# Kernel tuning notes

Hardware: AMD Instinct MI355X
Metric: run time of the kernel (lower is better)

Reference implementation:

```python
import jax, jax.numpy as jnp
import numpy as np

CCA_W, INTRA_W, AUX_W, OS_W, RFS_W = 0.1, 0.05, 1.0, 1.0, 1.0


def cox_loss(risk, events, times):
    # Efron-tied Cox partial likelihood, vectorized over tie groups.
    order = jnp.argsort(-times)  # descending time
    r = risk[order]
    e = events[order]
    t = times[order]
    B = r.shape[0]
    max_r = jnp.max(r)
    exp_r = jnp.exp(r - max_r)
    cum = jnp.cumsum(exp_r)  # risk-set sums (descending time => cumsum)
    # contiguous tie groups (times sorted, ties adjacent)
    new_grp = jnp.concatenate([jnp.zeros(1, jnp.int32), (t[1:] != t[:-1]).astype(jnp.int32)])
    gid = jnp.cumsum(new_grp)
    rss = jax.ops.segment_max(cum, gid, num_segments=B)[gid]          # cum_exp_risk at last idx of group
    tes = jax.ops.segment_sum(exp_r * e, gid, num_segments=B)[gid]     # tied exp-risk sum
    d = jax.ops.segment_sum(e, gid, num_segments=B)[gid]               # tie count (events)
    # rank l of each event within its tie group (0..d-1)
    c = jnp.cumsum(e)
    start = jax.ops.segment_min(jnp.arange(B), gid, num_segments=B)[gid]
    before = c[start] - e[start]
    l = c - 1.0 - before
    d_safe = jnp.where(d > 0, d, 1.0)
    denom = rss - (l / d_safe) * tes
    contrib = e * (r - jnp.log(denom + 1e-12) - max_r)
    n_events = jnp.sum(e)
    return -jnp.sum(contrib) / (n_events + 1e-12)


def distance_correlation_loss(za, zb):
    def dist(x):
        xx = jnp.sum(x * x, axis=1, keepdims=True)
        d2 = xx + xx.T - 2.0 * (x @ x.T)
        return jnp.sqrt(jnp.maximum(d2, 1e-8))
    def dc(D):
        return D - D.mean(axis=1, keepdims=True) - D.mean(axis=0, keepdims=True) + D.mean()
    A = dc(dist(za))
    Bm = dc(dist(zb))
    dcov = jnp.mean(A * Bm)
    va = jnp.mean(A * A)
    vb = jnp.mean(Bm * Bm)
    return 1.0 - dcov / jnp.sqrt(jnp.maximum(va * vb, 1e-8))


def setup_inputs() -> dict:
    key = jax.random.key(0)
    ks = jax.random.split(key, 10)
    B, D = 8192, 256
    return {
        'risk_os': jax.random.normal(ks[0], (B,), jnp.float32),
        'risk_rfs': jax.random.normal(ks[1], (B,), jnp.float32),
        'z_ct': jax.random.normal(ks[2], (B, D), jnp.float32),
        'z_wsi': jax.random.normal(ks[3], (B, D), jnp.float32),
        'intra_wsi': jax.random.uniform(ks[4], (), jnp.float32),
        'intra_ct': jax.random.uniform(ks[5], (), jnp.float32),
        'evt_os': jax.random.randint(ks[6], (B,), 0, 2, jnp.int32),
        'tm_os': jax.random.randint(ks[7], (B,), 0, 1000, jnp.int32),
        'evt_rfs': jax.random.randint(ks[8], (B,), 0, 2, jnp.int32),
        'tm_rfs': jax.random.randint(ks[9], (B,), 0, 1000, jnp.int32),
    }


def reference(risk_os, risk_rfs, z_ct, z_wsi, intra_wsi, intra_ct,
              evt_os, tm_os, evt_rfs, tm_rfs):
    l_os = cox_loss(risk_os, evt_os.astype(jnp.float32), tm_os.astype(jnp.float32))
    l_rfs = cox_loss(risk_rfs, evt_rfs.astype(jnp.float32), tm_rfs.astype(jnp.float32))
    l_cca = distance_correlation_loss(z_ct, z_wsi)
    l_intra = intra_wsi + intra_ct
    total = OS_W * l_os + RFS_W * l_rfs + AUX_W * (CCA_W * l_cca + INTRA_W * l_intra)
    return total
```

## Files before the change

kernel.cpp:

```cpp
#include <hip/hip_runtime.h>
#include <hip/hip_bf16.h>
#include <math.h>

typedef __attribute__((ext_vector_type(4))) float f32x4;
typedef __attribute__((ext_vector_type(4))) int int4v;

#define NBINS 1000

__device__ __forceinline__ void gl16(const void* g, void* l) {
  __builtin_amdgcn_global_load_lds(
      (const __attribute__((address_space(1))) unsigned int*)g,
      (__attribute__((address_space(3))) unsigned int*)l, 16, 0, 0);
}

__device__ __forceinline__ float fp8mag(unsigned b) {
  const int e = (b >> 3) & 15;
  const int m = b & 7;
  return e ? ldexpf((float)(8 + m), e - 10) : ldexpf((float)m, -9);
}

__global__ __launch_bounds__(256)
void prep_kernel(const float* __restrict__ za, const float* __restrict__ zb,
                 float* __restrict__ na, float* __restrict__ nb,
                 unsigned char* __restrict__ zpa, unsigned char* __restrict__ zpb,
                 int B, int D)
{
  const int row = blockIdx.x * 4 + (threadIdx.x >> 6);
  const int lane = threadIdx.x & 63;
  const float* src; float* dst; unsigned char* bd; int r;
  if (row < B) { src = za; dst = na; bd = zpa; r = row; }
  else         { src = zb; dst = nb; bd = zpb; r = row - B; }
  const int rr = r & 127;
  const int sw = (rr >> 1) & 3;
  const size_t tbase = (size_t)(r >> 7) * 128 * D;
  float s = 0.f;
  for (int c = lane * 4; c < D; c += 256) {
    const f32x4 v = *(const f32x4*)&src[(size_t)r * D + c];
    unsigned u = (unsigned)__builtin_amdgcn_cvt_pk_fp8_f32(v[0], v[1], 0, false);
    u = (unsigned)__builtin_amdgcn_cvt_pk_fp8_f32(v[2], v[3], (int)u, true);
    const int sc = c >> 6;
    const int half = (c >> 5) & 1;
    const int kg = (c >> 3) & 3;
    const int rem = c & 7;
    const int slot = kg ^ sw;
    *(unsigned*)&bd[tbase + sc * 8192 + rr * 64 + slot * 16 + half * 8 + rem] = u;
    const float x0 = fp8mag(u & 255), x1 = fp8mag((u >> 8) & 255);
    const float x2 = fp8mag((u >> 16) & 255), x3 = fp8mag(u >> 24);
    s += x0 * x0 + x1 * x1 + x2 * x2 + x3 * x3;
  }
#pragma unroll
  for (int off = 32; off; off >>= 1) s += __shfl_xor(s, off);
  if (lane == 0) dst[r] = s;
}

__global__ __launch_bounds__(512, 2)
void dcor_kernel(const unsigned char* __restrict__ zpa,
                 const unsigned char* __restrict__ zpb,
                 const float* __restrict__ na, const float* __restrict__ nb,
                 float* __restrict__ Ra, float* __restrict__ Rb,
                 double* __restrict__ scalPart,
                 const float* __restrict__ r0, const int* __restrict__ e0, const int* __restrict__ t0,
                 const float* __restrict__ r1, const int* __restrict__ e1, const int* __restrict__ t1,
                 float* __restrict__ coxo,
                 int nt, int B, int D)
{
  __shared__ __align__(16) union SU {
    unsigned char jbuf[2][16384];
    struct { float sS[NBINS], sT[NBINS], sDc[NBINS], sc0[NBINS], sc1[NBINS], red[16], red3[48]; } c;
  } u;

  const int tid = threadIdx.x;
  const int bid = blockIdx.x;

  if (bid < 2) {
    const float* risk = bid ? r1 : r0;
    const int* evt = bid ? e1 : e0;
    const int* tm  = bid ? t1 : t0;
    const int NT = 512;

    float m = -3.0e38f;
    for (int i = tid; i < B; i += NT) m = fmaxf(m, risk[i]);
#pragma unroll
    for (int off = 32; off; off >>= 1) m = fmaxf(m, __shfl_xor(m, off));
    if ((tid & 63) == 0) u.c.red[tid >> 6] = m;
    __syncthreads();
    if (tid == 0) {
      float mm = u.c.red[0];
      for (int wv = 1; wv < 8; ++wv) mm = fmaxf(mm, u.c.red[wv]);
      u.c.red[0] = mm;
    }
    __syncthreads();
    const float maxr = u.c.red[0];

    for (int i = tid; i < NBINS; i += NT) { u.c.sS[i] = 0.f; u.c.sT[i] = 0.f; u.c.sDc[i] = 0.f; }
    __syncthreads();

    float sr = 0.f, nev = 0.f;
    for (int i = tid; i < B; i += NT) {
      const float r = risk[i];
      int t = tm[i];
      t = t < 0 ? 0 : (t >= NBINS ? NBINS - 1 : t);
      const float ex = expf(r - maxr);
      atomicAdd(&u.c.sS[t], ex);
      if (evt[i]) {
        atomicAdd(&u.c.sT[t], ex);
        atomicAdd(&u.c.sDc[t], 1.0f);
        sr += r; nev += 1.0f;
      }
    }
    __syncthreads();

    for (int i = tid; i < NBINS; i += NT) u.c.sc0[i] = u.c.sS[i];
    __syncthreads();
    float* pin = u.c.sc0; float* pout = u.c.sc1;
    for (int off = 1; off < NBINS; off <<= 1) {
      for (int i = tid; i < NBINS; i += NT) {
        float v = pin[i];
        if (i + off < NBINS) v += pin[i + off];
        pout[i] = v;
      }
      __syncthreads();
      float* tmp = pin; pin = pout; pout = tmp;
    }

    float ls = 0.f;
    for (int t = tid; t < NBINS; t += NT) {
      const float d = u.c.sDc[t];
      if (d > 0.f) {
        const float tes = u.c.sT[t];
        const float rs = pin[t];
        for (float l = 0.f; l < d - 0.5f; l += 1.f)
          ls += logf(rs - (l / d) * tes + 1e-12f);
      }
    }

    float v1 = sr, v2 = nev, v3 = ls;
#pragma unroll
    for (int off = 32; off; off >>= 1) {
      v1 += __shfl_xor(v1, off); v2 += __shfl_xor(v2, off); v3 += __shfl_xor(v3, off);
    }
    if ((tid & 63) == 0) { int wv = tid >> 6; u.c.red3[wv] = v1; u.c.red3[16 + wv] = v2; u.c.red3[32 + wv] = v3; }
    __syncthreads();
    if (tid == 0) {
      float SR = 0.f, NEV = 0.f, LS = 0.f;
      for (int wv = 0; wv < 8; ++wv) { SR += u.c.red3[wv]; NEV += u.c.red3[16 + wv]; LS += u.c.red3[32 + wv]; }
      coxo[bid] = -(SR - LS - NEV * maxr) / (NEV + 1e-12f);
    }
    return;
  }

  const int lane = tid & 63;
  const int w = tid >> 6;
  const int p = bid - 2;

  const int xcd = p & 7, pos = p >> 3;
  const int q = (xcd < 6 ? xcd * 32 : 192 + (xcd - 6) * 31) + pos;
  const int start = (q < 48) ? 9 * q : 432 + 8 * (q - 48);
  const int cnt = (q < 48) ? 9 : 8;

  const double tn = (double)(2 * nt + 1);
  int ib0 = (int)((tn - sqrt(tn * tn - 8.0 * (double)start)) * 0.5);
  if (ib0 < 0) ib0 = 0;
  if (ib0 > nt - 1) ib0 = nt - 1;
  while (((ib0 + 1) * nt - ((ib0 + 1) * ib0) / 2) <= start) ++ib0;
  while ((ib0 * nt - (ib0 * (ib0 - 1)) / 2) > start) --ib0;
  const int jb0 = ib0 + (start - (ib0 * nt - (ib0 * (ib0 - 1)) / 2));

  const int wr = w >> 1, wc = w & 1;
  const int lrow = lane & 15;
  const int kg = lane >> 4;
  const int kgx = kg ^ ((lrow >> 1) & 3);
  const int abase = (wr * 32 + lrow) * 64 + kgx * 16;
  const int bbase = (wc * 64 + lrow) * 64 + kgx * 16;

  union I4L { int4v v; long l[2]; };

  int cib = ib0, cjb = jb0;
  const unsigned char* pAi = zpa + (size_t)cib * 32768;
  const unsigned char* pBi = zpb + (size_t)cib * 32768;
  const unsigned char* gAj = zpa + (size_t)cjb * 32768;
  const unsigned char* gBj = zpb + (size_t)cjb * 32768;

  I4L iA[2][4], iB[2][4];
#pragma unroll
  for (int m2 = 0; m2 < 2; ++m2)
#pragma unroll
    for (int sc = 0; sc < 4; ++sc) {
      iA[m2][sc].v = *(const int4v*)(pAi + sc * 8192 + abase + m2 * 1024);
      iB[m2][sc].v = *(const int4v*)(pBi + sc * 8192 + abase + m2 * 1024);
    }

#define STAGEJ(par_, pa_, pb_, sc_) do {                              \
    const size_t co_ = (size_t)(sc_) * 8192 + w * 1024 + lane * 16;   \
    gl16((pa_) + co_, &u.jbuf[par_][w * 1024]);                       \
    gl16((pb_) + co_, &u.jbuf[par_][8192 + w * 1024]);                \
  } while (0)

  const f32x4 Z4 = {0.f, 0.f, 0.f, 0.f};
  f32x4 accA[2][4], accB[2][4];
#pragma unroll
  for (int m2 = 0; m2 < 2; ++m2)
#pragma unroll
    for (int n2 = 0; n2 < 4; ++n2) { accA[m2][n2] = Z4; accB[m2][n2] = Z4; }

  double dp0 = 0.0, dp1 = 0.0, dp2 = 0.0;

  STAGEJ(0, gAj, gBj, 0);
  STAGEJ(1, gAj, gBj, 1);

  for (int t = 0; t < cnt; ++t) {
    const unsigned char* nAj = gAj;
    const unsigned char* nBj = gBj;
#pragma unroll
    for (int sc = 0; sc < 4; ++sc) {
      if (t == cnt - 1 && sc == 3) asm volatile("s_waitcnt vmcnt(0)" ::: "memory");
      else                         asm volatile("s_waitcnt vmcnt(2)" ::: "memory");
      __builtin_amdgcn_sched_barrier(0);
      __builtin_amdgcn_s_barrier();
      __builtin_amdgcn_sched_barrier(0);

      {
        const unsigned char* jb = &u.jbuf[sc & 1][0];
        I4L bA[4], bB[4];
#pragma unroll
        for (int n2 = 0; n2 < 4; ++n2) bA[n2].v = *(const int4v*)&jb[bbase + n2 * 1024];
#pragma unroll
        for (int n2 = 0; n2 < 4; ++n2) bB[n2].v = *(const int4v*)&jb[8192 + bbase + n2 * 1024];
        __builtin_amdgcn_s_setprio(1);
#pragma unroll
        for (int m2 = 0; m2 < 2; ++m2)
#pragma unroll
          for (int n2 = 0; n2 < 4; ++n2) {
            accA[m2][n2] = __builtin_amdgcn_mfma_f32_16x16x32_fp8_fp8(iA[m2][sc].l[0], bA[n2].l[0], accA[m2][n2], 0, 0, 0);
            accA[m2][n2] = __builtin_amdgcn_mfma_f32_16x16x32_fp8_fp8(iA[m2][sc].l[1], bA[n2].l[1], accA[m2][n2], 0, 0, 0);
          }
#pragma unroll
        for (int m2 = 0; m2 < 2; ++m2)
#pragma unroll
          for (int n2 = 0; n2 < 4; ++n2) {
            accB[m2][n2] = __builtin_amdgcn_mfma_f32_16x16x32_fp8_fp8(iB[m2][sc].l[0], bB[n2].l[0], accB[m2][n2], 0, 0, 0);
            accB[m2][n2] = __builtin_amdgcn_mfma_f32_16x16x32_fp8_fp8(iB[m2][sc].l[1], bB[n2].l[1], accB[m2][n2], 0, 0, 0);
          }
        __builtin_amdgcn_s_setprio(0);
      }

      __builtin_amdgcn_sched_barrier(0);
      __builtin_amdgcn_s_barrier();
      __builtin_amdgcn_sched_barrier(0);

      if (sc == 0)      STAGEJ(0, gAj, gBj, 2);
      else if (sc == 1) STAGEJ(1, gAj, gBj, 3);
      else if (sc == 2) {
        if (t + 1 < cnt) {
          int njb = cjb + 1, nib = cib;
          if (njb == nt) { ++nib; njb = nib; }
          nAj = zpa + (size_t)njb * 32768;
          nBj = zpb + (size_t)njb * 32768;
          STAGEJ(0, nAj, nBj, 0);
        }
      } else {
        if (t + 1 < cnt) STAGEJ(1, nAj, nBj, 1);
      }
    }

    {
      const bool offd = (cjb != cib);
      const float fac = offd ? 2.0f : 1.0f;
      float pab = 0.f, paa = 0.f, pbb = 0.f;
      float rsa[2][4], rsb[2][4];
      float csa[4] = {0.f, 0.f, 0.f, 0.f}, csb[4] = {0.f, 0.f, 0.f, 0.f};
#pragma unroll
      for (int m2 = 0; m2 < 2; ++m2)
#pragma unroll
        for (int r = 0; r < 4; ++r) { rsa[m2][r] = 0.f; rsb[m2][r] = 0.f; }

      const int gi0 = cib * 128 + wr * 32;
      const int gj0 = cjb * 128 + wc * 64;

#pragma unroll
      for (int m2 = 0; m2 < 2; ++m2) {
        const int gr = gi0 + m2 * 16 + kg * 4;
        const f32x4 nai = *(const f32x4*)&na[gr];
        const f32x4 nbi = *(const f32x4*)&nb[gr];
#pragma unroll
        for (int n2 = 0; n2 < 4; ++n2) {
          const int gc = gj0 + n2 * 16 + lrow;
          const float naj = na[gc];
          const float nbj = nb[gc];
          const f32x4 ga = accA[m2][n2];
          const f32x4 gb = accB[m2][n2];
#pragma unroll
          for (int r = 0; r < 4; ++r) {
            const float d2a = fmaxf(nai[r] + naj - 2.0f * ga[r], 1e-8f);
            const float d2b = fmaxf(nbi[r] + nbj - 2.0f * gb[r], 1e-8f);
            const float Da = __builtin_amdgcn_sqrtf(d2a);
            const float Db = __builtin_amdgcn_sqrtf(d2b);
            pab += Da * Db;
            paa += d2a;
            pbb += d2b;
            rsa[m2][r] += Da;
            rsb[m2][r] += Db;
            csa[n2] += Da;
            csb[n2] += Db;
          }
        }
      }

#pragma unroll
      for (int m2 = 0; m2 < 2; ++m2)
#pragma unroll
        for (int r = 0; r < 4; ++r) {
          float va = rsa[m2][r], vb = rsb[m2][r];
          va += __shfl_xor(va, 1); va += __shfl_xor(va, 2); va += __shfl_xor(va, 4); va += __shfl_xor(va, 8);
          vb += __shfl_xor(vb, 1); vb += __shfl_xor(vb, 2); vb += __shfl_xor(vb, 4); vb += __shfl_xor(vb, 8);
          if (lrow == 0) {
            const int gi = gi0 + m2 * 16 + kg * 4 + r;
            atomicAdd(&Ra[gi], va);
            atomicAdd(&Rb[gi], vb);
          }
        }

      if (offd) {
#pragma unroll
        for (int n2 = 0; n2 < 4; ++n2) {
          float va = csa[n2], vb = csb[n2];
          va += __shfl_xor(va, 16); va += __shfl_xor(va, 32);
          vb += __shfl_xor(vb, 16); vb += __shfl_xor(vb, 32);
          if (kg == 0) {
            const int gj = gj0 + n2 * 16 + lrow;
            atomicAdd(&Ra[gj], va);
            atomicAdd(&Rb[gj], vb);
          }
        }
      }

      float q1 = fac * pab, q2 = fac * paa, q3 = fac * pbb;
#pragma unroll
      for (int off = 32; off; off >>= 1) {
        q1 += __shfl_xor(q1, off); q2 += __shfl_xor(q2, off); q3 += __shfl_xor(q3, off);
      }
      dp0 += (double)q1; dp1 += (double)q2; dp2 += (double)q3;
    }

    const int oldib = cib;
    if (++cjb == nt) { ++cib; cjb = cib; }
    gAj = zpa + (size_t)cjb * 32768;
    gBj = zpb + (size_t)cjb * 32768;
    if (cib != oldib && t + 1 < cnt) {
      pAi = zpa + (size_t)cib * 32768;
      pBi = zpb + (size_t)cib * 32768;
#pragma unroll
      for (int m2 = 0; m2 < 2; ++m2)
#pragma unroll
        for (int sc = 0; sc < 4; ++sc) {
          iA[m2][sc].v = *(const int4v*)(pAi + sc * 8192 + abase + m2 * 1024);
          iB[m2][sc].v = *(const int4v*)(pBi + sc * 8192 + abase + m2 * 1024);
        }
    }
#pragma unroll
    for (int m2 = 0; m2 < 2; ++m2)
#pragma unroll
      for (int n2 = 0; n2 < 4; ++n2) { accA[m2][n2] = Z4; accB[m2][n2] = Z4; }
  }
#undef STAGEJ

  if (lane == 0) {
    double* sp = scalPart + (size_t)(p * 8 + w) * 3;
    sp[0] = dp0; sp[1] = dp1; sp[2] = dp2;
  }
}

__global__ __launch_bounds__(256)
void finalize_kernel(const float* __restrict__ Ra, const float* __restrict__ Rb,
                     const double* __restrict__ scalPart, int NS,
                     const float* __restrict__ coxo,
                     const float* __restrict__ iw, const float* __restrict__ ic,
                     float* __restrict__ out, int B)
{
  const int tid = threadIdx.x;
  double v[8];
#pragma unroll
  for (int k = 0; k < 8; ++k) v[k] = 0.0;
  for (int i = tid; i < B; i += 256) {
    const double a = Ra[i], b = Rb[i];
    v[0] += a; v[1] += b; v[2] += a * b; v[3] += a * a; v[4] += b * b;
  }
  for (int i = tid; i < NS; i += 256) {
    const double* sp = scalPart + (size_t)i * 3;
    v[5] += sp[0]; v[6] += sp[1]; v[7] += sp[2];
  }
#pragma unroll
  for (int k = 0; k < 8; ++k)
#pragma unroll
    for (int off = 32; off; off >>= 1) v[k] += __shfl_xor(v[k], off);
  __shared__ double sred[32];
  const int w = tid >> 6;
  if ((tid & 63) == 0) {
#pragma unroll
    for (int k = 0; k < 8; ++k) sred[k * 4 + w] = v[k];
  }
  __syncthreads();
  if (tid == 0) {
    double r[8];
#pragma unroll
    for (int k = 0; k < 8; ++k) r[k] = sred[k * 4] + sred[k * 4 + 1] + sred[k * 4 + 2] + sred[k * 4 + 3];
    const double ta = r[0], tb = r[1], sab = r[2], saa = r[3], sbb = r[4];
    const double Pab = r[5], Paa = r[6], Pbb = r[7];
    const double n = (double)B;
    const double Sab = Pab - (2.0 / n) * sab + ta * tb / (n * n);
    const double Saa = Paa - (2.0 / n) * saa + ta * ta / (n * n);
    const double Sbb = Pbb - (2.0 / n) * sbb + tb * tb / (n * n);
    const double dcov = Sab / (n * n);
    const double va = Saa / (n * n);
    const double vb = Sbb / (n * n);
    const double l_cca = 1.0 - dcov / sqrt(fmax(va * vb, 1e-8));
    const double total = (double)coxo[0] + (double)coxo[1]
                       + (0.1 * l_cca + 0.05 * ((double)iw[0] + (double)ic[0]));
    out[0] = (float)total;
  }
}

extern "C" void kernel_launch(void* const* d_in, const int* in_sizes, int n_in,
                              void* d_out, int out_size, void* d_ws, size_t ws_size,
                              hipStream_t stream)
{
  (void)n_in; (void)out_size; (void)ws_size;
  const float* risk_os   = (const float*)d_in[0];
  const float* risk_rfs  = (const float*)d_in[1];
  const float* z_ct      = (const float*)d_in[2];
  const float* z_wsi     = (const float*)d_in[3];
  const float* intra_wsi = (const float*)d_in[4];
  const float* intra_ct  = (const float*)d_in[5];
  const int* evt_os  = (const int*)d_in[6];
  const int* tm_os   = (const int*)d_in[7];
  const int* evt_rfs = (const int*)d_in[8];
  const int* tm_rfs  = (const int*)d_in[9];

  const int B = in_sizes[0];
  const int D = in_sizes[2] / B;
  const int nt = B / 128;
  const int NS = 254 * 8;

  float* ws = (float*)d_ws;
  float* Ra = ws;
  float* Rb = ws + B;
  float* coxo = ws + 2 * B;
  float* na  = ws + 2 * B + 16;
  float* nbv = ws + 3 * B + 16;
  double* scalPart = (double*)(ws + 4 * B + 16);
  unsigned char* zpa = (unsigned char*)(ws + 4 * B + 16 + 6 * NS + 8);
  unsigned char* zpb = zpa + (size_t)B * D;

  (void)hipMemsetAsync(d_ws, 0, (size_t)(2 * B) * sizeof(float), stream);

  prep_kernel<<<(2 * B) / 4, 256, 0, stream>>>(z_ct, z_wsi, na, nbv, zpa, zpb, B, D);
  dcor_kernel<<<256, 512, 0, stream>>>(zpa, zpb, na, nbv, Ra, Rb, scalPart,
                                       risk_os, evt_os, tm_os, risk_rfs, evt_rfs, tm_rfs,
                                       coxo, nt, B, D);
  finalize_kernel<<<1, 256, 0, stream>>>(Ra, Rb, scalPart, NS, coxo, intra_wsi, intra_ct, (float*)d_out, B);
}
```

Before: 89.85 us.

## Triple-buffer LDS staging to drop second barrier per k-chunk

Replaces the double-buffered j-tile staging with a three-slot ring buffer in LDS. Each k-chunk now has a single barrier instead of two, and the prefetch of the chunk two steps ahead is issued right after that barrier, before the MFMA work. This removes one workgroup barrier per chunk and gives the global-to-LDS loads more time to overlap with compute. It costs an extra 16KB of LDS, which may lower occupancy at two blocks per CU, and the wait counts must stay correct for the new prefetch distance.

```diff
diff --git a/kernel.cpp b/kernel.cpp
--- a/kernel.cpp
+++ b/kernel.cpp
@@ -65,7 +65,7 @@
                  int nt, int B, int D)
 {
   __shared__ __align__(16) union SU {
-    unsigned char jbuf[2][16384];
+    unsigned char jbuf[3][16384];
     struct { float sS[NBINS], sT[NBINS], sDc[NBINS], sc0[NBINS], sc1[NBINS], red[16], red3[48]; } c;
   } u;
 
@@ -176,10 +176,11 @@
   union I4L { int4v v; long l[2]; };
 
   int cib = ib0, cjb = jb0;
+  int ssib = ib0, ssjb = jb0;
   const unsigned char* pAi = zpa + (size_t)cib * 32768;
   const unsigned char* pBi = zpb + (size_t)cib * 32768;
-  const unsigned char* gAj = zpa + (size_t)cjb * 32768;
-  const unsigned char* gBj = zpb + (size_t)cjb * 32768;
+  const unsigned char* sAj = zpa + (size_t)ssjb * 32768;
+  const unsigned char* sBj = zpb + (size_t)ssjb * 32768;
 
   I4L iA[2][4], iB[2][4];
 #pragma unroll
@@ -190,11 +191,8 @@
       iB[m2][sc].v = *(const int4v*)(pBi + sc * 8192 + abase + m2 * 1024);
     }
 
-#define STAGEJ(par_, pa_, pb_, sc_) do {                              \
-    const size_t co_ = (size_t)(sc_) * 8192 + w * 1024 + lane * 16;   \
-    gl16((pa_) + co_, &u.jbuf[par_][w * 1024]);                       \
-    gl16((pb_) + co_, &u.jbuf[par_][8192 + w * 1024]);                \
-  } while (0)
+  const int lgofs = w * 1024 + lane * 16;
+  const int llofs = w * 1024;
 
   const f32x4 Z4 = {0.f, 0.f, 0.f, 0.f};
   f32x4 accA[2][4], accB[2][4];
@@ -205,12 +203,15 @@
 
   double dp0 = 0.0, dp1 = 0.0, dp2 = 0.0;
 
-  STAGEJ(0, gAj, gBj, 0);
-  STAGEJ(1, gAj, gBj, 1);
+  gl16(sAj + 0 * 8192 + lgofs, &u.jbuf[0][llofs]);
+  gl16(sBj + 0 * 8192 + lgofs, &u.jbuf[0][8192 + llofs]);
+  gl16(sAj + 1 * 8192 + lgofs, &u.jbuf[1][llofs]);
+  gl16(sBj + 1 * 8192 + lgofs, &u.jbuf[1][8192 + llofs]);
+
+  int bufc = 0;
+  int bufs = 2;
 
   for (int t = 0; t < cnt; ++t) {
-    const unsigned char* nAj = gAj;
-    const unsigned char* nBj = gBj;
 #pragma unroll
     for (int sc = 0; sc < 4; ++sc) {
       if (t == cnt - 1 && sc == 3) asm volatile("s_waitcnt vmcnt(0)" ::: "memory");
@@ -219,13 +220,24 @@
       __builtin_amdgcn_s_barrier();
       __builtin_amdgcn_sched_barrier(0);
 
+      if (t + 1 < cnt || sc < 2) {
+        if (sc == 2) {
+          if (++ssjb == nt) { ++ssib; ssjb = ssib; }
+          sAj = zpa + (size_t)ssjb * 32768;
+          sBj = zpb + (size_t)ssjb * 32768;
+        }
+        const size_t co = (size_t)((sc + 2) & 3) * 8192 + lgofs;
+        gl16(sAj + co, &u.jbuf[bufs][llofs]);
+        gl16(sBj + co, &u.jbuf[bufs][8192 + llofs]);
+      }
+
       {
-        const unsigned char* jb = &u.jbuf[sc & 1][0];
+        const unsigned char* jb_ = &u.jbuf[bufc][0];
         I4L bA[4], bB[4];
 #pragma unroll
-        for (int n2 = 0; n2 < 4; ++n2) bA[n2].v = *(const int4v*)&jb[bbase + n2 * 1024];
-#pragma unroll
-        for (int n2 = 0; n2 < 4; ++n2) bB[n2].v = *(const int4v*)&jb[8192 + bbase + n2 * 1024];
+        for (int n2 = 0; n2 < 4; ++n2) bA[n2].v = *(const int4v*)&jb_[bbase + n2 * 1024];
+#pragma unroll
+        for (int n2 = 0; n2 < 4; ++n2) bB[n2].v = *(const int4v*)&jb_[8192 + bbase + n2 * 1024];
         __builtin_amdgcn_s_setprio(1);
 #pragma unroll
         for (int m2 = 0; m2 < 2; ++m2)
@@ -244,23 +256,8 @@
         __builtin_amdgcn_s_setprio(0);
       }
 
-      __builtin_amdgcn_sched_barrier(0);
-      __builtin_amdgcn_s_barrier();
-      __builtin_amdgcn_sched_barrier(0);
-
-      if (sc == 0)      STAGEJ(0, gAj, gBj, 2);
-      else if (sc == 1) STAGEJ(1, gAj, gBj, 3);
-      else if (sc == 2) {
-        if (t + 1 < cnt) {
-          int njb = cjb + 1, nib = cib;
-          if (njb == nt) { ++nib; njb = nib; }
-          nAj = zpa + (size_t)njb * 32768;
-          nBj = zpb + (size_t)njb * 32768;
-          STAGEJ(0, nAj, nBj, 0);
-        }
-      } else {
-        if (t + 1 < cnt) STAGEJ(1, nAj, nBj, 1);
-      }
+      bufc = (bufc == 2) ? 0 : bufc + 1;
+      bufs = (bufs == 2) ? 0 : bufs + 1;
     }
 
     {
@@ -344,8 +341,6 @@
 
     const int oldib = cib;
     if (++cjb == nt) { ++cib; cjb = cib; }
-    gAj = zpa + (size_t)cjb * 32768;
-    gBj = zpb + (size_t)cjb * 32768;
     if (cib != oldib && t + 1 < cnt) {
       pAi = zpa + (size_t)cib * 32768;
       pBi = zpb + (size_t)cib * 32768;
@@ -362,7 +357,6 @@
 #pragma unroll
       for (int n2 = 0; n2 < 4; ++n2) { accA[m2][n2] = Z4; accB[m2][n2] = Z4; }
   }
-#undef STAGEJ
 
   if (lane == 0) {
     double* sp = scalPart + (size_t)(p * 8 + w) * 3;
```

After: 89.92 us. Within noise of the previous version (+0.1%).
